# Kernel tuning notes

Measured on AMD Instinct MI355X. Metric: run time of the kernel, lower is better.

Reference implementation:

```python
import jax, jax.numpy as jnp
import numpy as np
from jax import lax

G, K, C_IN, C_FEAT, H, W, B = 8, 6, 512, 256, 64, 64, 1


def apply_offset(offset):
    # offset: [N, 2, H, W] pixel-space offsets -> sampling grid [N, H, W, 2] in [-1, 1]
    # channel 0 displaces x (width), channel 1 displaces y (height), matching the
    # reversed-meshgrid logic of the original torch apply_offset.
    n, _, h, w = offset.shape
    jj = jnp.arange(w, dtype=offset.dtype)[None, None, :]
    ii = jnp.arange(h, dtype=offset.dtype)[None, :, None]
    gx = (jj + offset[:, 0]) / ((w - 1.0) / 2.0) - 1.0
    gy = (ii + offset[:, 1]) / ((h - 1.0) / 2.0) - 1.0
    return jnp.stack([gx, gy], axis=-1)


def grid_sample_border(img, grid):
    # img: [N, C, H, W], grid: [N, H, W, 2] in [-1, 1]
    # Bilinear, padding_mode='border', align_corners=False (torch grid_sample default).
    n, c, h, w = img.shape
    x = jnp.clip((grid[..., 0] + 1.0) * w * 0.5 - 0.5, 0.0, w - 1.0)
    y = jnp.clip((grid[..., 1] + 1.0) * h * 0.5 - 0.5, 0.0, h - 1.0)
    x0 = jnp.floor(x)
    y0 = jnp.floor(y)
    wx = (x - x0)[:, None]  # [N,1,H,W]
    wy = (y - y0)[:, None]
    x0i = x0.astype(jnp.int32)
    y0i = y0.astype(jnp.int32)
    x1i = jnp.minimum(x0i + 1, w - 1)
    y1i = jnp.minimum(y0i + 1, h - 1)

    def gather(im, yi, xi):  # im [C,H,W]; yi, xi [H,W]
        return im[:, yi, xi]

    g = jax.vmap(gather)
    v00 = g(img, y0i, x0i)
    v01 = g(img, y0i, x1i)
    v10 = g(img, y1i, x0i)
    v11 = g(img, y1i, x1i)
    return (1.0 - wy) * ((1.0 - wx) * v00 + wx * v01) + wy * ((1.0 - wx) * v10 + wx * v11)


def setup_inputs() -> dict:
    key = jax.random.key(0)
    ks = jax.random.split(key, 11)
    s = 0.02
    return {
        "gar_feat": jax.random.normal(ks[0], (B, C_FEAT, H, W), jnp.float32),
        "cond_feat": jax.random.normal(ks[1], (B, C_FEAT, H, W), jnp.float32),
        "mask": jax.random.uniform(ks[2], (B, G, C_FEAT), dtype=jnp.float32),
        "W1": jax.random.normal(ks[3], (G, 128, C_IN, 3, 3), jnp.float32) * s,
        "b1": jax.random.normal(ks[4], (G, 128), jnp.float32) * s,
        "W2": jax.random.normal(ks[5], (G, 64, 128, 3, 3), jnp.float32) * s,
        "b2": jax.random.normal(ks[6], (G, 64), jnp.float32) * s,
        "W3": jax.random.normal(ks[7], (G, 32, 64, 3, 3), jnp.float32) * s,
        "b3": jax.random.normal(ks[8], (G, 32), jnp.float32) * s,
        "W4": jax.random.normal(ks[9], (G, 3 * K, 32, 3, 3), jnp.float32) * s,
        "b4": jax.random.normal(ks[10], (G, 3 * K), jnp.float32) * s,
    }


def reference(gar_feat, cond_feat, mask, W1, b1, W2, b2, W3, b3, W4, b4):
    b, c, h, w = gar_feat.shape
    g = W1.shape[0]
    k = W4.shape[1] // 3
    inp = jnp.concatenate([gar_feat, cond_feat], axis=1)  # [B, 2C, H, W]

    def conv(x, wgt, bias):
        return lax.conv_general_dilated(
            x, wgt, (1, 1), 'SAME', dimension_numbers=('NCHW', 'OIHW', 'NCHW')
        ) + bias[None, :, None, None]

    def lrelu(x):
        return jnp.where(x >= 0, x, 0.1 * x)

    def group_net(w1, bb1, w2, bb2, w3, bb3, w4, bb4):
        hid = lrelu(conv(inp, w1, bb1))
        hid = lrelu(conv(hid, w2, bb2))
        hid = lrelu(conv(hid, w3, bb3))
        return conv(hid, w4, bb4)  # [B, 3k, H, W]

    oa = jax.vmap(group_net)(W1, b1, W2, b2, W3, b3, W4, b4)  # [G, B, 3k, H, W]
    attn = jax.nn.softmax(oa[:, :, 2 * k:], axis=0)           # softmax across groups: [G,B,k,H,W]
    off = oa[:, :, :2 * k].reshape(g, b * k, 2, h, w)
    grid = jax.vmap(apply_offset)(off)                        # [G, B*k, H, W, 2]

    rep = jnp.repeat(gar_feat, k, axis=0)                     # [B*k, C, H, W]

    def warp_group(grid_g, attn_g, mask_g):
        samp = grid_sample_border(rep, grid_g).reshape(b, k, c, h, w)
        wfeat = jnp.sum(samp * attn_g[:, :, None], axis=1)    # [B, C, H, W]
        return wfeat * mask_g[:, :, None, None]

    warped = jax.vmap(warp_group)(grid, attn, jnp.transpose(mask, (1, 0, 2)))
    return jnp.sum(warped, axis=0)  # [B, C, H, W]
```

## Files before the change

### kernel.cpp

```cpp
#include <hip/hip_runtime.h>
#include <hip/hip_bf16.h>

typedef __hip_bfloat16 bf16;
typedef unsigned short ushort8v __attribute__((ext_vector_type(8)));
typedef short  s16x4  __attribute__((ext_vector_type(4)));
typedef short  bf16x8 __attribute__((ext_vector_type(8)));
typedef float  f32x4  __attribute__((ext_vector_type(4)));

#define HW 4096
#define IMG_W 64

__device__ __forceinline__ float bfbits2f(unsigned short u) {
    return __uint_as_float(((unsigned int)u) << 16);
}
__device__ __forceinline__ short f2bs(float f) {
    bf16 h = __float2bfloat16(f);
    return *reinterpret_cast<short*>(&h);
}

__device__ __forceinline__ void gl_lds16(const void* g, void* s) {
    __builtin_amdgcn_global_load_lds(
        (const __attribute__((address_space(1))) unsigned int*)g,
        (__attribute__((address_space(3))) unsigned int*)s, 16, 0, 0);
}

__device__ void pack_input_dev(const float* __restrict__ gar,
                               const float* __restrict__ cond,
                               short* __restrict__ outp, int bx2, float* tile)
{
    int bx = bx2 & 127;
    int by = bx2 >> 7;
    int tx = threadIdx.x & 31;
    int ty = threadIdx.x >> 5;
#pragma unroll
    for (int i = 0; i < 4; ++i) {
        int c = by * 32 + ty + i * 8;
        const float* src = (c < 256) ? (gar + (size_t)c * HW)
                                     : (cond + (size_t)(c - 256) * HW);
        tile[(ty + i * 8) * 33 + tx] = src[bx * 32 + tx];
    }
    __syncthreads();
#pragma unroll
    for (int i = 0; i < 4; ++i) {
        int p = bx * 32 + ty + i * 8;
        outp[((size_t)by * 4096 + p) * 32 + tx] = f2bs(tile[tx * 33 + ty + i * 8]);
    }
}

template<int CIN, int CREAL, int BN, int NT, bool COAL>
__device__ void pack_w_dev(const float* __restrict__ wgt, char* __restrict__ wp,
                           int bx, short* sT)
{
    constexpr int NCC  = CIN / 32;
    constexpr int BLKB = 9 * 4 * BN * 16;

    const int t  = threadIdx.x;
    const int cc = bx % NCC;
    const int nt = (bx / NCC) % NT;
    const int g  = bx / (NT * NCC);

    for (int i = t; i < BLKB / 8; i += 256)
        reinterpret_cast<s16x4*>(sT)[i] = s16x4{0, 0, 0, 0};
    __syncthreads();

    int ocmax = CREAL - nt * BN; if (ocmax > BN) ocmax = BN;
    const size_t base = ((size_t)(g * CREAL + nt * BN) * CIN + cc * 32) * 9;
    for (int i = t; i < ocmax * 288; i += 256) {
        int oc = i / 288;
        int r  = i % 288;
        int ic = r / 9, tap = r % 9;
        size_t idx;
        if (COAL) idx = (size_t)(((tap * BN + oc) * 4 + (ic >> 3)) * 8 + (ic & 7));
        else      idx = (size_t)(((tap * 4 + (ic >> 3)) * BN + oc) * 8 + (ic & 7));
        sT[idx] = f2bs(wgt[base + (size_t)oc * CIN * 9 + r]);
    }
    __syncthreads();

    const s16x4* src = reinterpret_cast<const s16x4*>(sT);
    s16x4* dst = reinterpret_cast<s16x4*>(wp + (size_t)bx * BLKB);
    for (int i = t; i < BLKB / 8; i += 256)
        dst[i] = src[i];
}

__global__ __launch_bounds__(256)
void pack_all(const float* __restrict__ gar, const float* __restrict__ cond,
              const float* __restrict__ W1, const float* __restrict__ W2,
              const float* __restrict__ W3, const float* __restrict__ W4,
              short* inp_t, char* W1p, char* W2p, char* W3p, char* W4p)
{
    __shared__ __align__(16) short sbuf[9 * 4 * 64 * 8];
    int bx = blockIdx.x;
    if (bx < 256)      pack_w_dev<512, 128, 64, 2, true >(W1, W1p, bx,       sbuf);
    else if (bx < 288) pack_w_dev<128,  64, 64, 1, false>(W2, W2p, bx - 256, sbuf);
    else if (bx < 304) pack_w_dev< 64,  32, 32, 1, false>(W3, W3p, bx - 288, sbuf);
    else if (bx < 312) pack_w_dev< 32,  18, 32, 1, false>(W4, W4p, bx - 304, sbuf);
    else pack_input_dev(gar, cond, inp_t, bx - 312, (float*)sbuf);
}

template<int ICP, int CREAL, int BN, int ROWS, int OF, int NT, int NW, int PIPE,
         bool PIXMAJ_OUT, bool LEAKY, bool OUT_F32>
__global__ __launch_bounds__(NW * 64, 2)
void conv_mfma(const short* __restrict__ inp, const char* __restrict__ wp,
               const float* __restrict__ bias, void* __restrict__ outv)
{
    constexpr int NCC  = ICP / 32;
    constexpr int HALO = ROWS + 2;
    constexpr int NPT  = 4096 / (ROWS * 64);
    constexpr int BLKB = 9 * 4 * BN * 16;
    constexpr int RNDS = BLKB / 1024;
    constexpr int NBUF = (PIPE && NCC > 1) ? 2 : 1;
    constexpr int SMAX = (HALO + NW - 1) / NW;

    __shared__ __align__(16) short sA[HALO][4][68][8];
    __shared__ __align__(16) char  sBraw[NBUF][BLKB];

    const int b  = blockIdx.x;
    const int g  = b & 7;
    const int r_ = b >> 3;
    const int pt = r_ % NPT;
    const int nt = r_ / NPT;
    const int r0 = pt * ROWS;

    const int t    = threadIdx.x;
    const int wave = t >> 6, lane = t & 63;
    const int l15  = lane & 15, quad = lane >> 4;

    int row_l, ocw;
    if (NW == 8) {
        if (ROWS == 4) { row_l = wave >> 1; ocw = (wave & 1) * (BN / 2); }
        else           { row_l = wave >> 2; ocw = (wave & 3) * (BN / 4); }
    } else {
        row_l = (ROWS == 4) ? wave : (wave & 1);
        ocw   = (ROWS == 4) ? 0 : (wave >> 1) * (BN / 2);
    }

    const size_t gpix = (ICP == 512) ? 0 : ((size_t)g * 4096);
    const char*  wb   = wp + (size_t)((g * NT + nt) * NCC) * BLKB;

    const int acol = t & 63;
    const int r2   = t >> 6;

    bf16x8 pre[SMAX][4];

    auto stageA_load = [&](int cc) {
#pragma unroll
        for (int s = 0; s < SMAX; ++s) {
            int j = r2 + s * NW;
            if (j < HALO) {
                int gy = r0 - 1 + j;
                if (gy >= 0 && gy < 64) {
                    const short* sp = inp + ((gpix + gy * 64 + acol) * ICP + cc * 32);
#pragma unroll
                    for (int q = 0; q < 4; ++q)
                        pre[s][q] = *reinterpret_cast<const bf16x8*>(sp + q * 8);
                } else {
#pragma unroll
                    for (int q = 0; q < 4; ++q)
                        pre[s][q] = bf16x8{0, 0, 0, 0, 0, 0, 0, 0};
                }
            }
        }
    };
    auto stageA_write = [&]() {
#pragma unroll
        for (int s = 0; s < SMAX; ++s) {
            int j = r2 + s * NW;
            if (j < HALO) {
#pragma unroll
                for (int q = 0; q < 4; ++q)
                    *reinterpret_cast<bf16x8*>(&sA[j][q][acol + 1][0]) = pre[s][q];
            }
        }
    };
    auto stageB = [&](int cc) {
        const char* wsrc = wb + (size_t)cc * BLKB;
        char* sbb = (char*)sBraw[(NBUF == 2) ? (cc & 1) : 0];
        for (int r = wave; r < RNDS; r += NW)
            gl_lds16(wsrc + r * 1024 + lane * 16, sbb + r * 1024);
    };

    f32x4 acc[OF][4];
#pragma unroll
    for (int o = 0; o < OF; ++o)
#pragma unroll
        for (int p = 0; p < 4; ++p)
#pragma unroll
            for (int r = 0; r < 4; ++r) acc[o][p][r] = 0.f;

    if (t < HALO * 8) {
        int row = t >> 3, q = (t >> 1) & 3, cp = (t & 1) ? 65 : 0;
        *reinterpret_cast<bf16x8*>(&sA[row][q][cp][0]) =
            bf16x8{0, 0, 0, 0, 0, 0, 0, 0};
    }

    stageB(0);
    stageA_load(0);
    stageA_write();

    for (int cc = 0; cc < NCC; ++cc) {
        __syncthreads();
        if (cc + 1 < NCC) {
            if (PIPE) stageB(cc + 1);
            stageA_load(cc + 1);
        }
        const bf16x8* sBv = reinterpret_cast<const bf16x8*>(
            sBraw[(NBUF == 2) ? (cc & 1) : 0]);

#pragma unroll
        for (int dy = 0; dy < 3; ++dy) {
#pragma unroll
            for (int dx = 0; dx < 3; ++dx) {
                bf16x8 pF[4];
#pragma unroll
                for (int p = 0; p < 4; ++p)
                    pF[p] = *reinterpret_cast<const bf16x8*>(
                        &sA[row_l + dy][quad][p * 16 + l15 + dx][0]);
                bf16x8 wF[OF];
#pragma unroll
                for (int o = 0; o < OF; ++o)
                    wF[o] = sBv[((dy * 3 + dx) * 4 + quad) * BN + ocw + o * 16 + l15];
#pragma unroll
                for (int o = 0; o < OF; ++o)
#pragma unroll
                    for (int p = 0; p < 4; ++p)
                        acc[o][p] = __builtin_amdgcn_mfma_f32_16x16x32_bf16(
                            wF[o], pF[p], acc[o][p], 0, 0, 0);
            }
        }
        __syncthreads();
        if (cc + 1 < NCC) {
            if (!PIPE) stageB(cc + 1);
            stageA_write();
        }
    }

    const int prow = r0 + row_l;
#pragma unroll
    for (int o = 0; o < OF; ++o)
#pragma unroll
        for (int reg = 0; reg < 4; ++reg) {
            const int ocl = ocw + o * 16 + quad * 4 + reg;
            const int ocg = nt * BN + ocl;
            if (ocg < CREAL) {
                const float bv = bias[g * CREAL + ocg];
                if (PIXMAJ_OUT) {
                    short* outp = (short*)outv;
                    const size_t pixbase = ((size_t)g * 4096 + prow * 64);
#pragma unroll
                    for (int p = 0; p < 4; ++p) {
                        float v = acc[o][p][reg] + bv;
                        if (LEAKY) v = v >= 0.f ? v : 0.1f * v;
                        outp[(pixbase + p * 16 + l15) * (NT * BN) + ocg] = f2bs(v);
                    }
                } else if (OUT_F32) {
                    float* outp = (float*)outv;
                    const size_t base = ((size_t)(g * CREAL + ocg)) * HW + prow * IMG_W;
#pragma unroll
                    for (int p = 0; p < 4; ++p) {
                        float v = acc[o][p][reg] + bv;
                        if (LEAKY) v = v >= 0.f ? v : 0.1f * v;
                        outp[base + p * 16 + l15] = v;
                    }
                } else {
                    short* outp = (short*)outv;
                    const size_t base = ((size_t)(g * CREAL + ocg)) * HW + prow * IMG_W;
#pragma unroll
                    for (int p = 0; p < 4; ++p) {
                        float v = acc[o][p][reg] + bv;
                        if (LEAKY) v = v >= 0.f ? v : 0.1f * v;
                        outp[base + p * 16 + l15] = f2bs(v);
                    }
                }
            }
        }
}

__global__ __launch_bounds__(512, 2)
void conv1_p2(const short* __restrict__ inp, const char* __restrict__ wp,
              const float* __restrict__ bias, short* __restrict__ outp)
{
    __shared__ __align__(16) short sA[2][4][66][4][8];

    const int b  = blockIdx.x;
    const int g  = b & 7;
    const int pt = b >> 3;
    const int r0 = pt * 2;

    const int t    = threadIdx.x;
    const int wave = t >> 6, lane = t & 63;
    const int l15  = lane & 15, quad = lane >> 4;

    const int row_l = wave & 1;
    const int ocq   = wave >> 1;
    const int ntw   = ocq >> 1;
    const int ocw64 = (ocq & 1) * 32;

    const short* wb    = (const short*)wp + (size_t)(g * 2 + ntw) * 16 * 18432;
    const short* wlane = wb + ((size_t)(ocw64 + l15) * 4 + quad) * 8;

    auto stageDMA = [&](int cc, int buf) {
        const int row = wave >> 1;
        const int gy  = r0 - 1 + row;
        if (gy >= 0 && gy < 64) {
            const short* src = inp + ((size_t)cc * 4096 + (size_t)gy * 64) * 32
                                   + (size_t)lane * 8;
            const int c4 = (wave & 1) * 2;
            gl_lds16(src + c4 * 512,       &sA[buf][row][1 + c4 * 16][0][0]);
            gl_lds16(src + (c4 + 1) * 512, &sA[buf][row][1 + (c4 + 1) * 16][0][0]);
        }
    };

    f32x4 acc[2][4];
#pragma unroll
    for (int o = 0; o < 2; ++o)
#pragma unroll
        for (int f = 0; f < 4; ++f)
#pragma unroll
            for (int r = 0; r < 4; ++r) acc[o][f][r] = 0.f;

    stageDMA(0, 0);
    if (t < 64) {
        int buf = t >> 5, row = (t >> 3) & 3, q = (t >> 1) & 3;
        int col = (t & 1) ? 65 : 0;
        *reinterpret_cast<bf16x8*>(&sA[buf][row][col][q][0]) =
            bf16x8{0, 0, 0, 0, 0, 0, 0, 0};
    }
    if (r0 == 0 || r0 == 62) {
        int zr = (r0 == 0) ? 0 : 3;
        for (int i = t; i < 2 * 66 * 4; i += 512) {
            int buf = i / 264, rem = i % 264;
            *reinterpret_cast<bf16x8*>(&sA[buf][zr][rem >> 2][rem & 3][0]) =
                bf16x8{0, 0, 0, 0, 0, 0, 0, 0};
        }
    }

    bf16x8 w[2][2];
    bf16x8 pf[2][4];
#pragma unroll
    for (int o = 0; o < 2; ++o)
        w[0][o] = *reinterpret_cast<const bf16x8*>(wlane + o * 512);

    auto body = [&](int cc, int cur, int par) {
        const short* wcc = wlane + (size_t)cc * 18432;
        __syncthreads();
        if (cc + 1 < 16) stageDMA(cc + 1, cur ^ 1);
#pragma unroll
        for (int f = 0; f < 4; ++f)
            pf[0][f] = *reinterpret_cast<const bf16x8*>(
                &sA[cur][row_l][f * 16 + l15][quad][0]);
#pragma unroll
        for (int tap = 0; tap < 9; ++tap) {
            const int pb = tap & 1, pn = pb ^ 1;
            const int cb = (tap + par) & 1, nb = cb ^ 1;
            if (tap < 8) {
                const int dy1 = (tap + 1) / 3, dx1 = (tap + 1) % 3;
#pragma unroll
                for (int f = 0; f < 4; ++f)
                    pf[pn][f] = *reinterpret_cast<const bf16x8*>(
                        &sA[cur][row_l + dy1][f * 16 + l15 + dx1][quad][0]);
            }
            const short* nsrc = wcc + (size_t)(tap + 1) * 2048;
#pragma unroll
            for (int o = 0; o < 2; ++o)
                w[nb][o] = *reinterpret_cast<const bf16x8*>(nsrc + o * 512);
            __builtin_amdgcn_sched_barrier(0);
#pragma unroll
            for (int o = 0; o < 2; ++o)
#pragma unroll
                for (int f = 0; f < 4; ++f)
                    acc[o][f] = __builtin_amdgcn_mfma_f32_16x16x32_bf16(
                        w[cb][o], pf[pb][f], acc[o][f], 0, 0, 0);
        }
    };

    for (int c2 = 0; c2 < 16; c2 += 2) {
        body(c2,     0, 0);
        body(c2 + 1, 1, 1);
    }

    const int prow = r0 + row_l;
    const size_t pixbase = (size_t)g * 4096 + (size_t)prow * 64;
#pragma unroll
    for (int o = 0; o < 2; ++o)
#pragma unroll
        for (int reg = 0; reg < 4; ++reg) {
            const int ocg = ocq * 32 + o * 16 + quad * 4 + reg;
            const float bv = bias[g * 128 + ocg];
#pragma unroll
            for (int f = 0; f < 4; ++f) {
                float v = acc[o][f][reg] + bv;
                v = v >= 0.f ? v : 0.1f * v;
                outp[(pixbase + f * 16 + l15) * 128 + ocg] = f2bs(v);
            }
        }
}

__global__ __launch_bounds__(256)
void warp_combine_kernel(const float* __restrict__ oa,
                         const short* __restrict__ inp_t,
                         const float* __restrict__ mask,
                         float* __restrict__ out)
{
    __shared__ __align__(16) float4 sWts[8][6][8];
    __shared__ __align__(16) int4   sIdx[8][6][8];

    const int t = threadIdx.x;

    if (t < 48) {
        int lp = t / 6;
        int k  = t % 6;
        int p  = blockIdx.x * 8 + lp;
        int x  = p & 63, y = p >> 6;

        float l[8];
        float m = -1e30f;
#pragma unroll
        for (int g = 0; g < 8; ++g) {
            l[g] = oa[(size_t)(g * 18 + 12 + k) * HW + p];
            m = fmaxf(m, l[g]);
        }
        float s = 0.f;
#pragma unroll
        for (int g = 0; g < 8; ++g) { l[g] = __expf(l[g] - m); s += l[g]; }
        float inv = 1.f / s;

#pragma unroll
        for (int g = 0; g < 8; ++g) {
            float a  = l[g] * inv;
            float ox = oa[(size_t)(g * 18 + 2 * k)     * HW + p];
            float oy = oa[(size_t)(g * 18 + 2 * k + 1) * HW + p];
            float sx = fminf(fmaxf(((float)x + ox) * (64.f / 63.f) - 0.5f, 0.f), 63.f);
            float sy = fminf(fmaxf(((float)y + oy) * (64.f / 63.f) - 0.5f, 0.f), 63.f);
            float fx0 = floorf(sx), fy0 = floorf(sy);
            int   x0 = (int)fx0,    y0i = (int)fy0;
            float wx = sx - fx0,    wy = sy - fy0;
            int   x1 = min(x0 + 1, 63), y1 = min(y0i + 1, 63);
            sWts[lp][k][g] = make_float4(a * (1.f - wy) * (1.f - wx),
                                         a * (1.f - wy) * wx,
                                         a * wy * (1.f - wx),
                                         a * wy * wx);
            sIdx[lp][k][g] = make_int4(y0i * 64 + x0, y0i * 64 + x1,
                                       y1  * 64 + x0, y1  * 64 + x1);
        }
    }
    __syncthreads();

    const int lp = t >> 5;
    const int p  = blockIdx.x * 8 + lp;
    const int c0 = (t & 31) * 8;
    const short* ipc = inp_t + (size_t)(c0 >> 5) * (4096 * 32) + (c0 & 31);

    float acc[8];
#pragma unroll
    for (int j = 0; j < 8; ++j) acc[j] = 0.f;

    for (int g = 0; g < 8; ++g) {
        float4 m0 = *reinterpret_cast<const float4*>(mask + g * 256 + c0);
        float4 m1 = *reinterpret_cast<const float4*>(mask + g * 256 + c0 + 4);
        float mk[8] = {m0.x, m0.y, m0.z, m0.w, m1.x, m1.y, m1.z, m1.w};
#pragma unroll
        for (int k = 0; k < 6; ++k) {
            float4 w  = sWts[lp][k][g];
            int4   id = sIdx[lp][k][g];
            ushort8v v00 = *reinterpret_cast<const ushort8v*>(ipc + (size_t)id.x * 32);
            ushort8v v01 = *reinterpret_cast<const ushort8v*>(ipc + (size_t)id.y * 32);
            ushort8v v10 = *reinterpret_cast<const ushort8v*>(ipc + (size_t)id.z * 32);
            ushort8v v11 = *reinterpret_cast<const ushort8v*>(ipc + (size_t)id.w * 32);
#pragma unroll
            for (int j = 0; j < 8; ++j) {
                float sv = w.x * bfbits2f(v00[j]) + w.y * bfbits2f(v01[j])
                         + w.z * bfbits2f(v10[j]) + w.w * bfbits2f(v11[j]);
                acc[j] = fmaf(mk[j], sv, acc[j]);
            }
        }
    }
#pragma unroll
    for (int j = 0; j < 8; ++j)
        out[(size_t)(c0 + j) * HW + p] = acc[j];
}

extern "C" void kernel_launch(void* const* d_in, const int* in_sizes, int n_in,
                              void* d_out, int out_size, void* d_ws, size_t ws_size,
                              hipStream_t stream)
{
    (void)in_sizes; (void)n_in; (void)out_size; (void)ws_size;
    const float* gar  = (const float*)d_in[0];
    const float* cond = (const float*)d_in[1];
    const float* mask = (const float*)d_in[2];
    const float* W1   = (const float*)d_in[3];
    const float* b1   = (const float*)d_in[4];
    const float* W2   = (const float*)d_in[5];
    const float* b2   = (const float*)d_in[6];
    const float* W3   = (const float*)d_in[7];
    const float* b3   = (const float*)d_in[8];
    const float* W4   = (const float*)d_in[9];
    const float* b4   = (const float*)d_in[10];
    float* out = (float*)d_out;

    char* ws = (char*)d_ws;
    short* inp_t  = (short*)(ws);
    char*  W1p    = ws + (4u << 20);
    short* hid2_t = (short*)(ws + (4u << 20));
    short* hid3_t = (short*)(ws + (8u << 20));
    float* oa     = (float*)(ws + (10u << 20) + (512u << 10));
    char*  W2p    = ws + (14u << 20);
    char*  W3p    = ws + (15u << 20) + (512u << 10);
    char*  W4p    = ws + (16u << 20);
    short* hid1_t = (short*)(ws + (17u << 20));

    pack_all<<<2360, 256, 0, stream>>>(gar, cond, W1, W2, W3, W4,
                                       inp_t, W1p, W2p, W3p, W4p);

    conv1_p2<<<256, 512, 0, stream>>>(inp_t, W1p, b1, hid1_t);
    conv_mfma<128, 64, 64, 2, 1, 1, 8, 1, true, true, false>
        <<<256, 512, 0, stream>>>(hid1_t, W2p, b2, hid2_t);
    conv_mfma<64, 32, 32, 2, 1, 1, 4, 1, true, true, false>
        <<<256, 256, 0, stream>>>(hid2_t, W3p, b3, hid3_t);
    conv_mfma<32, 18, 32, 2, 1, 1, 4, 1, false, false, true>
        <<<256, 256, 0, stream>>>(hid3_t, W4p, b4, oa);

    warp_combine_kernel<<<512, 256, 0, stream>>>(oa, inp_t, mask, out);
}
```

Measured before the change: 199.8 us.

## Add dedicated conv2 kernel with DMA staging and channel-blocked hid1 layout

Replaces the generic conv2 launch with a specialized conv2_p2 kernel that stages channel-blocked input rows into LDS through global_load_lds DMA, double-buffered across the four input-channel chunks. conv1 now writes hid1 in a [chunk][pixel][32] layout to feed this kernel, and W2 is packed in the coalesced order. Separately, the input pack also writes a pixel-major [pixel][256] bf16 copy of gar_feat, so the warp-combine gathers read contiguous 16-byte rows. The cost is an extra workspace buffer and extra writes in the pack kernel.

Measured after the change: 200.4 us. About the same (+0.3%).

```diff
diff --git a/kernel.cpp b/kernel.cpp
--- a/kernel.cpp
+++ b/kernel.cpp
@@ -26,7 +26,8 @@
 
 __device__ void pack_input_dev(const float* __restrict__ gar,
                                const float* __restrict__ cond,
-                               short* __restrict__ outp, int bx2, float* tile)
+                               short* __restrict__ outp,
+                               short* __restrict__ gart, int bx2, float* tile)
 {
     int bx = bx2 & 127;
     int by = bx2 >> 7;
@@ -43,7 +44,10 @@
 #pragma unroll
     for (int i = 0; i < 4; ++i) {
         int p = bx * 32 + ty + i * 8;
-        outp[((size_t)by * 4096 + p) * 32 + tx] = f2bs(tile[tx * 33 + ty + i * 8]);
+        short v = f2bs(tile[tx * 33 + ty + i * 8]);
+        outp[((size_t)by * 4096 + p) * 32 + tx] = v;
+        if (by < 8)
+            gart[(size_t)p * 256 + by * 32 + tx] = v;
     }
 }
 
@@ -86,15 +90,16 @@
 void pack_all(const float* __restrict__ gar, const float* __restrict__ cond,
               const float* __restrict__ W1, const float* __restrict__ W2,
               const float* __restrict__ W3, const float* __restrict__ W4,
-              short* inp_t, char* W1p, char* W2p, char* W3p, char* W4p)
+              short* inp_t, short* gar_t,
+              char* W1p, char* W2p, char* W3p, char* W4p)
 {
     __shared__ __align__(16) short sbuf[9 * 4 * 64 * 8];
     int bx = blockIdx.x;
     if (bx < 256)      pack_w_dev<512, 128, 64, 2, true >(W1, W1p, bx,       sbuf);
-    else if (bx < 288) pack_w_dev<128,  64, 64, 1, false>(W2, W2p, bx - 256, sbuf);
+    else if (bx < 288) pack_w_dev<128,  64, 64, 1, true >(W2, W2p, bx - 256, sbuf);
     else if (bx < 304) pack_w_dev< 64,  32, 32, 1, false>(W3, W3p, bx - 288, sbuf);
     else if (bx < 312) pack_w_dev< 32,  18, 32, 1, false>(W4, W4p, bx - 304, sbuf);
-    else pack_input_dev(gar, cond, inp_t, bx - 312, (float*)sbuf);
+    else pack_input_dev(gar, cond, inp_t, gar_t, bx - 312, (float*)sbuf);
 }
 
 template<int ICP, int CREAL, int BN, int ROWS, int OF, int NT, int NW, int PIPE,
@@ -386,18 +391,129 @@
         for (int reg = 0; reg < 4; ++reg) {
             const int ocg = ocq * 32 + o * 16 + quad * 4 + reg;
             const float bv = bias[g * 128 + ocg];
+            const size_t cbase = (size_t)(ocg >> 5) * 32768;
+            const int cin = ocg & 31;
 #pragma unroll
             for (int f = 0; f < 4; ++f) {
                 float v = acc[o][f][reg] + bv;
                 v = v >= 0.f ? v : 0.1f * v;
-                outp[(pixbase + f * 16 + l15) * 128 + ocg] = f2bs(v);
-            }
-        }
+                outp[(cbase + pixbase + f * 16 + l15) * 32 + cin] = f2bs(v);
+            }
+        }
+}
+
+__global__ __launch_bounds__(512, 2)
+void conv2_p2(const short* __restrict__ inp, const char* __restrict__ wp,
+              const float* __restrict__ bias, short* __restrict__ outp)
+{
+    __shared__ __align__(16) short sA[2][4][66][4][8];
+
+    const int b  = blockIdx.x;
+    const int g  = b & 7;
+    const int pt = b >> 3;
+    const int r0 = pt * 2;
+
+    const int t    = threadIdx.x;
+    const int wave = t >> 6, lane = t & 63;
+    const int l15  = lane & 15, quad = lane >> 4;
+
+    const int row_l = wave & 1;
+    const int ocq   = wave >> 1;
+
+    const short* wb    = (const short*)wp + (size_t)g * 4 * 18432;
+    const short* wlane = wb + ((size_t)(ocq * 16 + l15) * 4 + quad) * 8;
+
+    auto stageDMA = [&](int cc, int buf) {
+        const int row = wave >> 1;
+        const int gy  = r0 - 1 + row;
+        if (gy >= 0 && gy < 64) {
+            const short* src = inp + ((size_t)cc * 32768 + (size_t)g * 4096
+                                      + (size_t)gy * 64) * 32
+                                   + (size_t)lane * 8;
+            const int c4 = (wave & 1) * 2;
+            gl_lds16(src + c4 * 512,       &sA[buf][row][1 + c4 * 16][0][0]);
+            gl_lds16(src + (c4 + 1) * 512, &sA[buf][row][1 + (c4 + 1) * 16][0][0]);
+        }
+    };
+
+    f32x4 acc[4];
+#pragma unroll
+    for (int f = 0; f < 4; ++f)
+#pragma unroll
+        for (int r = 0; r < 4; ++r) acc[f][r] = 0.f;
+
+    stageDMA(0, 0);
+    if (t < 64) {
+        int buf = t >> 5, row = (t >> 3) & 3, q = (t >> 1) & 3;
+        int col = (t & 1) ? 65 : 0;
+        *reinterpret_cast<bf16x8*>(&sA[buf][row][col][q][0]) =
+            bf16x8{0, 0, 0, 0, 0, 0, 0, 0};
+    }
+    if (r0 == 0 || r0 == 62) {
+        int zr = (r0 == 0) ? 0 : 3;
+        for (int i = t; i < 2 * 66 * 4; i += 512) {
+            int buf = i / 264, rem = i % 264;
+            *reinterpret_cast<bf16x8*>(&sA[buf][zr][rem >> 2][rem & 3][0]) =
+                bf16x8{0, 0, 0, 0, 0, 0, 0, 0};
+        }
+    }
+
+    bf16x8 w[2];
+    bf16x8 pf[2][4];
+    w[0] = *reinterpret_cast<const bf16x8*>(wlane);
+
+    auto body = [&](int cc, int cur, int par) {
+        const short* wcc = wlane + (size_t)cc * 18432;
+        __syncthreads();
+        if (cc + 1 < 4) stageDMA(cc + 1, cur ^ 1);
+#pragma unroll
+        for (int f = 0; f < 4; ++f)
+            pf[0][f] = *reinterpret_cast<const bf16x8*>(
+                &sA[cur][row_l][f * 16 + l15][quad][0]);
+#pragma unroll
+        for (int tap = 0; tap < 9; ++tap) {
+            const int pb = tap & 1, pn = pb ^ 1;
+            const int cb = (tap + par) & 1, nb = cb ^ 1;
+            if (tap < 8) {
+                const int dy1 = (tap + 1) / 3, dx1 = (tap + 1) % 3;
+#pragma unroll
+                for (int f = 0; f < 4; ++f)
+                    pf[pn][f] = *reinterpret_cast<const bf16x8*>(
+                        &sA[cur][row_l + dy1][f * 16 + l15 + dx1][quad][0]);
+            }
+            w[nb] = *reinterpret_cast<const bf16x8*>(
+                wcc + (size_t)(tap + 1) * 2048);
+            __builtin_amdgcn_sched_barrier(0);
+#pragma unroll
+            for (int f = 0; f < 4; ++f)
+                acc[f] = __builtin_amdgcn_mfma_f32_16x16x32_bf16(
+                    w[cb], pf[pb][f], acc[f], 0, 0, 0);
+        }
+    };
+
+    for (int c2 = 0; c2 < 4; c2 += 2) {
+        body(c2,     0, 0);
+        body(c2 + 1, 1, 1);
+    }
+
+    const int prow = r0 + row_l;
+    const size_t pixbase = (size_t)g * 4096 + (size_t)prow * 64;
+#pragma unroll
+    for (int reg = 0; reg < 4; ++reg) {
+        const int ocg = ocq * 16 + quad * 4 + reg;
+        const float bv = bias[g * 64 + ocg];
+#pragma unroll
+        for (int f = 0; f < 4; ++f) {
+            float v = acc[f][reg] + bv;
+            v = v >= 0.f ? v : 0.1f * v;
+            outp[(pixbase + f * 16 + l15) * 64 + ocg] = f2bs(v);
+        }
+    }
 }
 
 __global__ __launch_bounds__(256)
 void warp_combine_kernel(const float* __restrict__ oa,
-                         const short* __restrict__ inp_t,
+                         const short* __restrict__ gar_t,
                          const float* __restrict__ mask,
                          float* __restrict__ out)
 {
@@ -448,7 +564,7 @@
     const int lp = t >> 5;
     const int p  = blockIdx.x * 8 + lp;
     const int c0 = (t & 31) * 8;
-    const short* ipc = inp_t + (size_t)(c0 >> 5) * (4096 * 32) + (c0 & 31);
+    const short* ipc = gar_t + c0;
 
     float acc[8];
 #pragma unroll
@@ -462,10 +578,10 @@
         for (int k = 0; k < 6; ++k) {
             float4 w  = sWts[lp][k][g];
             int4   id = sIdx[lp][k][g];
-            ushort8v v00 = *reinterpret_cast<const ushort8v*>(ipc + (size_t)id.x * 32);
-            ushort8v v01 = *reinterpret_cast<const ushort8v*>(ipc + (size_t)id.y * 32);
-            ushort8v v10 = *reinterpret_cast<const ushort8v*>(ipc + (size_t)id.z * 32);
-            ushort8v v11 = *reinterpret_cast<const ushort8v*>(ipc + (size_t)id.w * 32);
+            ushort8v v00 = *reinterpret_cast<const ushort8v*>(ipc + (size_t)id.x * 256);
+            ushort8v v01 = *reinterpret_cast<const ushort8v*>(ipc + (size_t)id.y * 256);
+            ushort8v v10 = *reinterpret_cast<const ushort8v*>(ipc + (size_t)id.z * 256);
+            ushort8v v11 = *reinterpret_cast<const ushort8v*>(ipc + (size_t)id.w * 256);
 #pragma unroll
             for (int j = 0; j < 8; ++j) {
                 float sv = w.x * bfbits2f(v00[j]) + w.y * bfbits2f(v01[j])
@@ -507,17 +623,17 @@
     char*  W3p    = ws + (15u << 20) + (512u << 10);
     char*  W4p    = ws + (16u << 20);
     short* hid1_t = (short*)(ws + (17u << 20));
+    short* gar_t  = (short*)(ws + (26u << 20));
 
     pack_all<<<2360, 256, 0, stream>>>(gar, cond, W1, W2, W3, W4,
-                                       inp_t, W1p, W2p, W3p, W4p);
+                                       inp_t, gar_t, W1p, W2p, W3p, W4p);
 
     conv1_p2<<<256, 512, 0, stream>>>(inp_t, W1p, b1, hid1_t);
-    conv_mfma<128, 64, 64, 2, 1, 1, 8, 1, true, true, false>
-        <<<256, 512, 0, stream>>>(hid1_t, W2p, b2, hid2_t);
+    conv2_p2<<<256, 512, 0, stream>>>(hid1_t, W2p, b2, hid2_t);
     conv_mfma<64, 32, 32, 2, 1, 1, 4, 1, true, true, false>
         <<<256, 256, 0, stream>>>(hid2_t, W3p, b3, hid3_t);
     conv_mfma<32, 18, 32, 2, 1, 1, 4, 1, false, false, true>
         <<<256, 256, 0, stream>>>(hid3_t, W4p, b4, oa);
 
-    warp_combine_kernel<<<512, 256, 0, stream>>>(oa, inp_t, mask, out);
-}
+    warp_combine_kernel<<<512, 256, 0, stream>>>(oa, gar_t, mask, out);
+}
```
